# Optimization experiments

Hardware: AMD Instinct MI355X
Metric: run time of the kernel (lower is better)

The kernel has to match this reference:

```python
import jax, jax.numpy as jnp
import numpy as np

EMBED, HID, INSIDE, OUTSIDE, EPS = 128, 64, 4, 8, 1e-5
N_NODES, N_EDGES, BATCH, SEQLEN = 16384, 262144, 64, 21


def _layernorm(x, g, b):
    m = x.mean(-1, keepdims=True)
    v = ((x - m) ** 2).mean(-1, keepdims=True)
    return (x - m) * jax.lax.rsqrt(v + EPS) * g + b


def _lstm_dir(x, Wih, Whh, bih, bhh, reverse):
    # x: [B, L, D] -> h: [B, L, HID]; PyTorch gate order i,f,g,o
    pre = jnp.einsum('bld,gd->blg', x, Wih) + bih + bhh  # [B,L,4H]
    pre = jnp.swapaxes(pre, 0, 1)  # [L,B,4H]
    h0 = jnp.zeros((x.shape[0], HID), x.dtype)

    def step(carry, xt):
        h, c = carry
        gates = xt + h @ Whh.T
        i, f, g, o = jnp.split(gates, 4, axis=-1)
        c = jax.nn.sigmoid(f) * c + jax.nn.sigmoid(i) * jnp.tanh(g)
        h = jax.nn.sigmoid(o) * jnp.tanh(c)
        return (h, c), h

    _, hs = jax.lax.scan(step, (h0, h0), pre, reverse=reverse)
    return jnp.swapaxes(hs, 0, 1)


def setup_inputs():
    key = jax.random.key(0)
    ks = jax.random.split(key, 40)
    f = jnp.float32
    N, E, B, L, D = N_NODES, N_EDGES, BATCH, SEQLEN, EMBED

    def w(k, shape, fan_in):
        return jax.random.normal(k, shape, f) * (1.0 / np.sqrt(fan_in))

    inp = {
        'x': jax.random.normal(ks[0], (N, 2561), f),
        'edge_index': jax.random.randint(ks[1], (2, E), 0, N, jnp.int32),
        'edge_attr': jax.random.normal(ks[2], (E, 3), f),
        # sorted node->graph assignment; every graph id 0..B-1 present
        'batch': ((jnp.arange(N, dtype=jnp.int32) * B) // N).astype(jnp.int32),
        'hotslice': jax.random.normal(ks[3], (B, L, 28), f),
        # randn_like noise tensors from the torch forward, made explicit inputs
        'noise_seqy': jax.random.normal(ks[4], (B, L, D), f),
        'noise_seqz': jax.random.normal(ks[5], (B, L, D), f),
        'noise_sty': jax.random.normal(ks[6], (N, D), f),
        'noise_stz': jax.random.normal(ks[7], (N, D), f),
        # AttnNN params
        'W_esm': w(ks[8], (D, 2560), 2560), 'b_esm': jnp.zeros((D,), f),
        'W_node': w(ks[9], (D, D + 1), D + 1), 'b_node': jnp.zeros((D,), f),
        'W_seq': w(ks[10], (D, 28), 28), 'b_seq': jnp.zeros((D,), f),
        # SeqStructBlock params
        'ln_seq_g': jnp.ones((D,), f), 'ln_seq_b': jnp.zeros((D,), f),
        'ln_st_g': jnp.ones((D,), f), 'ln_st_b': jnp.zeros((D,), f),
        'W_in': w(ks[11], (D, 2 * D + 3), 2 * D + 3), 'b_in': jnp.zeros((D,), f),
        'W_out': w(ks[12], (D, 2 * D + 3), 2 * D + 3), 'b_out': jnp.zeros((D,), f),
        'Wih_f': w(ks[13], (4 * HID, D), HID), 'Whh_f': w(ks[14], (4 * HID, HID), HID),
        'bih_f': jnp.zeros((4 * HID,), f), 'bhh_f': jnp.zeros((4 * HID,), f),
        'Wih_b': w(ks[15], (4 * HID, D), HID), 'Whh_b': w(ks[16], (4 * HID, HID), HID),
        'bih_b': jnp.zeros((4 * HID,), f), 'bhh_b': jnp.zeros((4 * HID,), f),
        # BatchNorm1d (eval mode: running stats)
        'bn_g': jnp.ones((D,), f), 'bn_b': jnp.zeros((D,), f),
        'bn_rm': jnp.zeros((D,), f), 'bn_rv': jnp.ones((D,), f),
    }
    return inp


def reference(x, edge_index, edge_attr, batch, hotslice,
              noise_seqy, noise_seqz, noise_sty, noise_stz,
              W_esm, b_esm, W_node, b_node, W_seq, b_seq,
              ln_seq_g, ln_seq_b, ln_st_g, ln_st_b,
              W_in, b_in, W_out, b_out,
              Wih_f, Whh_f, bih_f, bhh_f, Wih_b, Whh_b, bih_b, bhh_b,
              bn_g, bn_b, bn_rm, bn_rv):
    N = x.shape[0]
    B = hotslice.shape[0]
    src, dst = edge_index[0, 0::2], edge_index[1, 0::2]
    ea_in, ea_out = edge_attr[1::2], edge_attr[0::2]

    def ss(seq, struct):
        # bidirectional LSTM + residual + LayerNorm (dropout = identity, eval)
        hf = _lstm_dir(seq, Wih_f, Whh_f, bih_f, bhh_f, False)
        hb = _lstm_dir(seq, Wih_b, Whh_b, bih_b, bhh_b, True)
        seq = _layernorm(seq + jnp.concatenate([hf, hb], -1), ln_seq_g, ln_seq_b)
        sn = struct
        fs, fd = sn[src], sn[dst]  # [E/2, 128] gathers
        gin = jax.nn.sigmoid(jnp.concatenate([fs, fd, ea_in], -1) @ W_in.T + b_in)
        struct = struct + jax.ops.segment_sum(gin * fd, src, num_segments=N)
        gout = jax.nn.sigmoid(jnp.concatenate([fs, fd, ea_out], -1) @ W_out.T + b_out)
        struct = struct + jax.ops.segment_sum(gout * fs, dst, num_segments=N)
        return seq, _layernorm(struct, ln_st_g, ln_st_b)

    seq0 = hotslice @ W_seq.T + b_seq                       # [B,L,128]
    esm = x[:, 1:] @ W_esm.T + b_esm                        # [N,128]
    struct0 = jnp.concatenate([esm, x[:, :1]], -1) @ W_node.T + b_node  # [N,128]

    def outer(carry):
        sy, sz, ty, tz = carry

        def inner(c, _):
            szc, tzc = c
            return ss(seq0 + sy + szc, struct0 + ty + tzc), None

        (sz, tz), _ = jax.lax.scan(inner, (sz, tz), None, length=INSIDE)
        sy, ty = ss(sy + sz, ty + tz)
        return (sy, sz, ty, tz)

    carry = (noise_seqy, noise_seqz, noise_sty, noise_stz)
    carry, _ = jax.lax.scan(lambda c, _: (outer(c), None), carry, None,
                            length=OUTSIDE - 1)
    sy, sz, ty, tz = outer(carry)

    # middleSelect picks the first node of each consecutive batch run;
    # batch is sorted with every graph id present -> run starts via searchsorted
    starts = jnp.searchsorted(batch, jnp.arange(B, dtype=batch.dtype))
    feat = sy[:, 10, :] + ty[starts]                        # [B,128]
    # BatchNorm1d, eval mode (running stats)
    return (feat - bn_rm) * jax.lax.rsqrt(bn_rv + EPS) * bn_g + bn_b
```

## Files before the change

### kernel.cpp

```cpp
#include <hip/hip_runtime.h>
#include <hip/hip_fp16.h>
#include <math.h>

#define D 128
#define G4 256
#define LSEQ 21
#define EPSF 1e-5f

typedef unsigned short u16;
typedef __attribute__((ext_vector_type(8))) short bf16x8;
typedef __attribute__((ext_vector_type(4))) float f32x4;
typedef __attribute__((ext_vector_type(2))) unsigned u32x2;
typedef __attribute__((ext_vector_type(4))) unsigned u32x4;

#define MFMA16(a,b,c) __builtin_amdgcn_mfma_f32_16x16x32_bf16(a,b,c,0,0,0)

__device__ __forceinline__ float sigf(float x){ return 1.0f/(1.0f+__expf(-x)); }
__device__ __forceinline__ u16 f2bf(float x){
  unsigned u = __float_as_uint(x);
  return (u16)((u + 0x7FFFu + ((u>>16)&1u)) >> 16);
}
__device__ __forceinline__ float bf2f(u16 h){ return __uint_as_float(((unsigned)h)<<16); }
__device__ __forceinline__ unsigned pack_h2(float a, float b){
  __half2 h = __floats2half2_rn(a, b);
  return *(unsigned*)&h;
}
__device__ __forceinline__ float2 unpack_h2(unsigned u){
  __half2 h = *(__half2*)&u;
  return __half22float2(h);
}
__device__ __forceinline__ u16 f2h(float v){ __half h = __float2half(v); return *(u16*)&h; }

__device__ __forceinline__ void edge_acc(u32x4 a, uint2 g, bool valid,
                                         float2 po2, float2 w0, float2 w1, float2 w2,
                                         float& ax, float& ay){
  float e0=__uint_as_float(a.y), e1=__uint_as_float(a.z), e2=__uint_as_float(a.w);
  float2 ps0 = unpack_h2(g.x);
  float2 ps1 = unpack_h2(g.y);
  float gx = po2.x + ps0.x + e0*w0.x + e1*w1.x + e2*w2.x;
  float gy = po2.y + ps1.x + e0*w0.y + e1*w1.y + e2*w2.y;
  float mm = valid ? 1.f : 0.f;
  ax = fmaf(ps0.y*mm, sigf(gx), ax);
  ay = fmaf(ps1.y*mm, sigf(gy), ay);
}

__global__ void k_misc(int* __restrict__ starts, const int* __restrict__ batch, int N, int Bb,
                       float* __restrict__ WEin, float* __restrict__ WEout,
                       const float* __restrict__ W_in, const float* __restrict__ W_out,
                       float* __restrict__ bsum_f, float* __restrict__ bsum_b,
                       const float* __restrict__ bih_f, const float* __restrict__ bhh_f,
                       const float* __restrict__ bih_b, const float* __restrict__ bhh_b){
  int tid = threadIdx.x;
  if (tid < Bb){
    int lo = 0, hi = N;
    while (lo < hi){ int m = (lo+hi)>>1; if (batch[m] < tid) lo = m+1; else hi = m; }
    starts[tid] = lo;
  }
  for (int i = tid; i < 384; i += 256){
    int t = i >> 7, j = i & 127;
    WEin [i] = W_in [(size_t)j*259 + 256 + t];
    WEout[i] = W_out[(size_t)j*259 + 256 + t];
  }
  if (tid < 256){
    bsum_f[tid] = bih_f[tid] + bhh_f[tid];
    bsum_b[tid] = bih_b[tid] + bhh_b[tid];
  }
}

__global__ void k_packB(u16* __restrict__ PB4h, u16* __restrict__ PB4l,
                        u16* __restrict__ PBnh, u16* __restrict__ PBnl,
                        u16* __restrict__ PBEh, u16* __restrict__ PBEl,
                        const float* __restrict__ W_in, const float* __restrict__ W_out,
                        const float* __restrict__ W_node, const float* __restrict__ W_esm){
  int idx = blockIdx.x*256 + threadIdx.x;
  if (idx < 65536){
    int j = idx&7, l=(idx>>3)&63, q=idx>>9;
    int ks = q&3, nt = q>>2;
    int c = nt*16 + (l&15);
    int k = ks*32 + ((l>>4)<<3) + j;
    float v;
    if (c < 128)      v = W_in [(size_t)c*259 + k];
    else if (c < 256) v = W_in [(size_t)(c-128)*259 + 128 + k];
    else if (c < 384) v = W_out[(size_t)(c-256)*259 + k];
    else              v = W_out[(size_t)(c-384)*259 + 128 + k];
    u16 h = f2bf(v);
    PB4h[idx] = h; PB4l[idx] = f2bf(v - bf2f(h));
  } else if (idx < 65536 + 16384){
    int p = idx - 65536;
    int j = p&7, l=(p>>3)&63, q=p>>9;
    int ks = q&3, nt = q>>2;
    int c = nt*16 + (l&15);
    int k = ks*32 + ((l>>4)<<3) + j;
    float v = W_node[(size_t)c*129 + k];
    u16 h = f2bf(v);
    PBnh[p] = h; PBnl[p] = f2bf(v - bf2f(h));
  } else if (idx < 65536 + 16384 + 327680){
    int p = idx - 81920;
    int j = p&7, l=(p>>3)&63, q=p>>9;
    int ks = q%80, nt = q/80;
    int c = nt*16 + (l&15);
    int k = ks*32 + ((l>>4)<<3) + j;
    float v = W_esm[(size_t)c*2560 + k];
    u16 h = f2bf(v);
    PBEh[p] = h; PBEl[p] = f2bf(v - bf2f(h));
  }
}

__global__ void k_seq0(float* __restrict__ seq0, const float* __restrict__ hot,
                       const float* __restrict__ W_seq, const float* __restrict__ b_seq){
  int row = blockIdx.x, j = threadIdx.x;
  const float* h = hot + (size_t)row*28;
  const float* w = W_seq + (size_t)j*28;
  float acc = b_seq[j];
  #pragma unroll
  for (int k = 0; k < 28; k++) acc += h[k]*w[k];
  seq0[(size_t)row*D + j] = acc;
}

__global__ __launch_bounds__(256) void k_esm2(float* __restrict__ struct0, const float* __restrict__ x,
    const u16* __restrict__ PBEh, const u16* __restrict__ PBEl,
    const u16* __restrict__ PBnh, const u16* __restrict__ PBnl,
    const float* __restrict__ b_esm, const float* __restrict__ W_node,
    const float* __restrict__ b_node){
  __shared__ union {
    struct { u16 xh[32*72], xl[32*72]; } p1;
    struct { u16 Ah[32*136], Al[32*136]; } p2;
  } uu;
  __shared__ float esmF[32*132];
  int tid = threadIdx.x;
  int r0 = blockIdx.x*32;
  int w = tid>>6, l = tid&63;
  f32x4 acc[2][2];
  #pragma unroll
  for (int a=0;a<2;a++)
    #pragma unroll
    for (int b=0;b<2;b++) acc[a][b] = (f32x4){0.f,0.f,0.f,0.f};

  float xv[8];
  int rr = tid >> 5, k2i = tid & 31;
  #pragma unroll
  for (int q = 0; q < 4; q++){
    const float* src = x + (size_t)(r0+rr+8*q)*2561 + 1 + k2i*2;
    xv[2*q]   = src[0];
    xv[2*q+1] = src[1];
  }
  for (int kc = 0; kc < 2560; kc += 64){
    __syncthreads();
    unsigned* xh32 = (unsigned*)uu.p1.xh;
    unsigned* xl32 = (unsigned*)uu.p1.xl;
    #pragma unroll
    for (int q = 0; q < 4; q++){
      float v0 = xv[2*q], v1 = xv[2*q+1];
      u16 h0 = f2bf(v0), h1 = f2bf(v1);
      u16 l0 = f2bf(v0 - bf2f(h0)), l1 = f2bf(v1 - bf2f(h1));
      int r = rr + 8*q;
      xh32[r*36 + k2i] = (unsigned)h0 | ((unsigned)h1 << 16);
      xl32[r*36 + k2i] = (unsigned)l0 | ((unsigned)l1 << 16);
    }
    __syncthreads();
    if (kc + 64 < 2560){
      #pragma unroll
      for (int q = 0; q < 4; q++){
        const float* src = x + (size_t)(r0+rr+8*q)*2561 + 1 + kc + 64 + k2i*2;
        xv[2*q]   = src[0];
        xv[2*q+1] = src[1];
      }
    }
    #pragma unroll
    for (int ks = 0; ks < 2; ks++){
      bf16x8 ah[2], al[2];
      #pragma unroll
      for (int rt = 0; rt < 2; rt++){
        int row = rt*16 + (l&15);
        int k = ks*32 + ((l>>4)<<3);
        ah[rt] = *(const bf16x8*)&uu.p1.xh[row*72 + k];
        al[rt] = *(const bf16x8*)&uu.p1.xl[row*72 + k];
      }
      int ksg = (kc>>5) + ks;
      #pragma unroll
      for (int ctl = 0; ctl < 2; ctl++){
        int nt = w*2 + ctl;
        bf16x8 bh = *(const bf16x8*)&PBEh[((size_t)(nt*80 + ksg)*64 + l)*8];
        bf16x8 bl = *(const bf16x8*)&PBEl[((size_t)(nt*80 + ksg)*64 + l)*8];
        #pragma unroll
        for (int rt = 0; rt < 2; rt++){
          acc[rt][ctl] = MFMA16(ah[rt], bh, acc[rt][ctl]);
          acc[rt][ctl] = MFMA16(al[rt], bh, acc[rt][ctl]);
          acc[rt][ctl] = MFMA16(ah[rt], bl, acc[rt][ctl]);
        }
      }
    }
  }
  __syncthreads();
  int cq = l & 15, rqb = (l>>4)*4;
  #pragma unroll
  for (int ctl = 0; ctl < 2; ctl++){
    int coln = (w*2+ctl)*16 + cq;
    float be = b_esm[coln];
    #pragma unroll
    for (int rt = 0; rt < 2; rt++)
      #pragma unroll
      for (int r = 0; r < 4; r++)
        esmF[(rt*16+rqb+r)*132 + coln] = acc[rt][ctl][r] + be;
  }
  __syncthreads();
  {
    unsigned* Ah32 = (unsigned*)uu.p2.Ah;
    unsigned* Al32 = (unsigned*)uu.p2.Al;
    int rr2 = tid >> 6, k2 = tid & 63;
    #pragma unroll
    for (int q = 0; q < 8; q++){
      int r = rr2 + 4*q;
      float v0 = esmF[r*132 + k2*2];
      float v1 = esmF[r*132 + k2*2 + 1];
      u16 h0 = f2bf(v0), h1 = f2bf(v1);
      u16 l0 = f2bf(v0 - bf2f(h0)), l1 = f2bf(v1 - bf2f(h1));
      Ah32[r*68 + k2] = (unsigned)h0 | ((unsigned)h1 << 16);
      Al32[r*68 + k2] = (unsigned)l0 | ((unsigned)l1 << 16);
    }
  }
  __syncthreads();
  f32x4 acc2[2][2];
  #pragma unroll
  for (int a=0;a<2;a++)
    #pragma unroll
    for (int b=0;b<2;b++) acc2[a][b] = (f32x4){0.f,0.f,0.f,0.f};
  #pragma unroll
  for (int ks = 0; ks < 4; ks++){
    bf16x8 ah[2], al[2];
    #pragma unroll
    for (int rt = 0; rt < 2; rt++){
      int row = rt*16 + (l&15);
      int k = ks*32 + ((l>>4)<<3);
      ah[rt] = *(const bf16x8*)&uu.p2.Ah[row*136 + k];
      al[rt] = *(const bf16x8*)&uu.p2.Al[row*136 + k];
    }
    #pragma unroll
    for (int ctl = 0; ctl < 2; ctl++){
      int nt = w*2 + ctl;
      bf16x8 bh = *(const bf16x8*)&PBnh[((size_t)(nt*4 + ks)*64 + l)*8];
      bf16x8 bl = *(const bf16x8*)&PBnl[((size_t)(nt*4 + ks)*64 + l)*8];
      #pragma unroll
      for (int rt = 0; rt < 2; rt++){
        acc2[rt][ctl] = MFMA16(ah[rt], bh, acc2[rt][ctl]);
        acc2[rt][ctl] = MFMA16(al[rt], bh, acc2[rt][ctl]);
        acc2[rt][ctl] = MFMA16(ah[rt], bl, acc2[rt][ctl]);
      }
    }
  }
  #pragma unroll
  for (int ctl = 0; ctl < 2; ctl++){
    int col = (w*2+ctl)*16 + cq;
    float wl = W_node[(size_t)col*129 + 128];
    float bn = b_node[col];
    #pragma unroll
    for (int rt = 0; rt < 2; rt++)
      #pragma unroll
      for (int r = 0; r < 4; r++){
        int row = r0 + rt*16 + rqb + r;
        float x0 = x[(size_t)row*2561];
        struct0[(size_t)row*D + col] = acc2[rt][ctl][r] + x0*wl + bn;
      }
  }
}

__global__ void k_zero2(int* a, int* b, int n){
  int i = blockIdx.x*blockDim.x + threadIdx.x;
  if (i < n){ a[i] = 0; b[i] = 0; }
}
__global__ void k_count(int* cnt_s, int* cnt_d, const int* __restrict__ ei, int E2){
  int e = blockIdx.x*blockDim.x + threadIdx.x;
  if (e < E2){
    atomicAdd(&cnt_s[ei[2*e]], 1);
    atomicAdd(&cnt_d[ei[2*E2 + 2*e]], 1);
  }
}
__global__ __launch_bounds__(1024) void k_scan(const int* __restrict__ cnt, int* __restrict__ offs, int n){
  __shared__ int sh[1024];
  __shared__ int sbase;
  int tid = threadIdx.x;
  if (tid == 0) sbase = 0;
  __syncthreads();
  for (int chunk = 0; chunk < n; chunk += 1024){
    int v = (chunk+tid < n) ? cnt[chunk+tid] : 0;
    sh[tid] = v;
    __syncthreads();
    for (int off = 1; off < 1024; off <<= 1){
      int t = (tid >= off) ? sh[tid-off] : 0;
      __syncthreads();
      sh[tid] += t;
      __syncthreads();
    }
    if (chunk+tid < n) offs[chunk+tid] = sbase + sh[tid] - v;
    __syncthreads();
    if (tid == 0) sbase += sh[1023];
    __syncthreads();
  }
  if (tid == 0) offs[n] = sbase;
}
__global__ void k_copy2(int* cur_s, const int* offs_s, int* cur_d, const int* offs_d, int n){
  int i = blockIdx.x*blockDim.x + threadIdx.x;
  if (i < n){ cur_s[i] = offs_s[i]; cur_d[i] = offs_d[i]; }
}
__global__ void k_fill(const int* __restrict__ ei, const float* __restrict__ eattr, int E2,
                       int* cur_s, int4* __restrict__ adj_s,
                       int* cur_d, int4* __restrict__ adj_d){
  int e = blockIdx.x*blockDim.x + threadIdx.x;
  if (e >= E2) return;
  int s = ei[2*e];
  int d = ei[2*E2 + 2*e];
  const float* ein  = eattr + (size_t)(2*e+1)*3;
  const float* eout = eattr + (size_t)(2*e)*3;
  int ps = atomicAdd(&cur_s[s], 1);
  adj_s[ps] = make_int4(d, __float_as_int(ein[0]),  __float_as_int(ein[1]),  __float_as_int(ein[2]));
  int pd = atomicAdd(&cur_d[d], 1);
  adj_d[pd] = make_int4(s, __float_as_int(eout[0]), __float_as_int(eout[1]), __float_as_int(eout[2]));
}
__global__ void k_pad(int4* __restrict__ adj_s, int4* __restrict__ adj_d, int E2){
  int t = threadIdx.x;
  if (t < 8){
    adj_s[E2+t] = make_int4(0,0,0,0);
    adj_d[E2+t] = make_int4(0,0,0,0);
  }
}

__global__ __launch_bounds__(256) void k_A(
  const float* __restrict__ s0t, const float* __restrict__ ty, const float* __restrict__ tz,
  float* __restrict__ struct_in,
  const u16* __restrict__ PB4h, const u16* __restrict__ PB4l,
  unsigned* __restrict__ G_in, unsigned* __restrict__ G_out,
  unsigned* __restrict__ PownPk,
  const float* __restrict__ b_in, const float* __restrict__ b_out,
  const float* __restrict__ s0s, const float* __restrict__ sy, const float* __restrict__ sz,
  float* __restrict__ seq_in, float* __restrict__ pre_f, float* __restrict__ pre_b,
  const float* __restrict__ Wih_f, const float* __restrict__ Wih_b,
  const float* __restrict__ bsum_f, const float* __restrict__ bsum_b,
  int N, int Bb)
{
  __shared__ union {
    struct { u16 Ah[32*136], Al[32*136]; float Sf[32*132]; } m;
    float sh[LSEQ*128];
  } u;
  int tid = threadIdx.x;
  if ((int)blockIdx.x >= Bb){
    int r0 = (blockIdx.x - Bb)*32;
    const float4* ty4 = (const float4*)(ty + (size_t)r0*D);
    const float4* tz4 = (const float4*)(tz + (size_t)r0*D);
    const float4* s04 = s0t ? (const float4*)(s0t + (size_t)r0*D) : nullptr;
    float4* si4 = (float4*)(struct_in + (size_t)r0*D);
    #pragma unroll
    for (int q = 0; q < 4; q++){
      int i = tid + 256*q;
      int r = i >> 5, k4 = i & 31;
      float4 v = ty4[i];
      float4 z = tz4[i];
      v.x += z.x; v.y += z.y; v.z += z.z; v.w += z.w;
      if (s04){ float4 s = s04[i]; v.x += s.x; v.y += s.y; v.z += s.z; v.w += s.w; }
      si4[i] = v;
      u16 h0 = f2bf(v.x), h1 = f2bf(v.y), h2 = f2bf(v.z), h3 = f2bf(v.w);
      *(ushort4*)&u.m.Ah[r*136 + k4*4] = make_ushort4(h0,h1,h2,h3);
      *(ushort4*)&u.m.Al[r*136 + k4*4] = make_ushort4(
          f2bf(v.x - bf2f(h0)), f2bf(v.y - bf2f(h1)),
          f2bf(v.z - bf2f(h2)), f2bf(v.w - bf2f(h3)));
      *(float4*)&u.m.Sf[r*132 + k4*4] = v;
    }
    __syncthreads();
    int w = tid >> 6, l = tid & 63;
    f32x4 acc[2][8];
    #pragma unroll
    for (int a=0;a<2;a++)
      #pragma unroll
      for (int b=0;b<8;b++) acc[a][b] = (f32x4){0.f,0.f,0.f,0.f};
    #pragma unroll
    for (int ks = 0; ks < 4; ks++){
      bf16x8 ah[2], al[2];
      #pragma unroll
      for (int rt = 0; rt < 2; rt++){
        int row = rt*16 + (l&15);
        int k = ks*32 + ((l>>4)<<3);
        ah[rt] = *(const bf16x8*)&u.m.Ah[row*136 + k];
        al[rt] = *(const bf16x8*)&u.m.Al[row*136 + k];
      }
      #pragma unroll
      for (int ct = 0; ct < 8; ct++){
        int nt = w*8 + ct;
        bf16x8 bh = *(const bf16x8*)&PB4h[((size_t)(nt*4 + ks)*64 + l)*8];
        bf16x8 bl = *(const bf16x8*)&PB4l[((size_t)(nt*4 + ks)*64 + l)*8];
        #pragma unroll
        for (int rt = 0; rt < 2; rt++){
          acc[rt][ct] = MFMA16(ah[rt], bh, acc[rt][ct]);
          acc[rt][ct] = MFMA16(al[rt], bh, acc[rt][ct]);
          acc[rt][ct] = MFMA16(ah[rt], bl, acc[rt][ct]);
        }
      }
    }
    __syncthreads();
    unsigned* stg = (unsigned*)u.m.Ah;
    u16* stg16 = (u16*)u.m.Ah;
    int cq = l & 15, rqb = (l>>4)*4;
    if (w == 1){
      #pragma unroll
      for (int ct = 0; ct < 8; ct++){
        int coln = ct*16 + cq;
        #pragma unroll
        for (int rt = 0; rt < 2; rt++){
          #pragma unroll
          for (int r = 0; r < 4; r++){
            int lr = rt*16 + rqb + r;
            stg[lr*128 + coln] = pack_h2(acc[rt][ct][r], u.m.Sf[lr*132 + coln]);
          }
        }
      }
    }
    __syncthreads();
    {
      uint4* dst = (uint4*)(G_in + (size_t)r0*D);
      const uint4* src = (const uint4*)stg;
      #pragma unroll
      for (int q = 0; q < 4; q++) dst[tid + 256*q] = src[tid + 256*q];
    }
    __syncthreads();
    if (w == 2){
      #pragma unroll
      for (int ct = 0; ct < 8; ct++){
        int coln = ct*16 + cq;
        #pragma unroll
        for (int rt = 0; rt < 2; rt++){
          #pragma unroll
          for (int r = 0; r < 4; r++){
            int lr = rt*16 + rqb + r;
            stg[lr*128 + coln] = pack_h2(acc[rt][ct][r], u.m.Sf[lr*132 + coln]);
          }
        }
      }
    }
    __syncthreads();
    {
      uint4* dst = (uint4*)(G_out + (size_t)r0*D);
      const uint4* src = (const uint4*)stg;
      #pragma unroll
      for (int q = 0; q < 4; q++) dst[tid + 256*q] = src[tid + 256*q];
    }
    __syncthreads();
    if (w == 0 || w == 3){
      const float* bb = (w == 0) ? b_in : b_out;
      int half = (w == 0) ? 0 : 1;
      #pragma unroll
      for (int ct = 0; ct < 8; ct++){
        int coln = ct*16 + cq;
        float bc = bb[coln];
        #pragma unroll
        for (int rt = 0; rt < 2; rt++){
          #pragma unroll
          for (int r = 0; r < 4; r++){
            int lr = rt*16 + rqb + r;
            stg16[(lr*128 + coln)*2 + half] = f2h(acc[rt][ct][r] + bc);
          }
        }
      }
    }
    __syncthreads();
    {
      uint4* dst = (uint4*)(PownPk + (size_t)r0*D);
      const uint4* src = (const uint4*)stg;
      #pragma unroll
      for (int q = 0; q < 4; q++) dst[tid + 256*q] = src[tid + 256*q];
    }
  } else {
    int b = blockIdx.x;
    for (int idx = tid; idx < LSEQ*128; idx += 256){
      size_t off = (size_t)b*LSEQ*128 + idx;
      float v = sy[off] + sz[off];
      if (s0s) v += s0s[off];
      u.sh[idx] = v;
      seq_in[off] = v;
    }
    __syncthreads();
    int g = tid;
    float accf[LSEQ], accb[LSEQ];
    float bf = bsum_f[g], bb = bsum_b[g];
    #pragma unroll
    for (int l = 0; l < LSEQ; l++){ accf[l] = bf; accb[l] = bb; }
    const float* wfp = Wih_f + (size_t)g*128;
    const float* wbp = Wih_b + (size_t)g*128;
    for (int kc = 0; kc < 128; kc += 16){
      float4 wf[4], wb[4];
      #pragma unroll
      for (int q = 0; q < 4; q++){
        wf[q] = *(const float4*)(wfp + kc + 4*q);
        wb[q] = *(const float4*)(wbp + kc + 4*q);
      }
      #pragma unroll
      for (int l = 0; l < LSEQ; l++){
        #pragma unroll
        for (int q = 0; q < 4; q++){
          float4 s4 = *(const float4*)&u.sh[l*128 + kc + 4*q];
          accf[l] += s4.x*wf[q].x + s4.y*wf[q].y + s4.z*wf[q].z + s4.w*wf[q].w;
          accb[l] += s4.x*wb[q].x + s4.y*wb[q].y + s4.z*wb[q].z + s4.w*wb[q].w;
        }
      }
    }
    for (int l = 0; l < LSEQ; l++){
      pre_f[((size_t)b*LSEQ + l)*G4 + g] = accf[l];
      pre_b[((size_t)b*LSEQ + l)*G4 + g] = accb[l];
    }
  }
}

__global__ __launch_bounds__(512) void k_B(
  const unsigned* __restrict__ G_in, const unsigned* __restrict__ G_out,
  const unsigned* __restrict__ PownPk,
  const float* __restrict__ struct_in, float* __restrict__ struct_out,
  const int* __restrict__ offs_s, const int4* __restrict__ adj_s,
  const int* __restrict__ offs_d, const int4* __restrict__ adj_d,
  const float* __restrict__ WEin, const float* __restrict__ WEout,
  const float* __restrict__ ln_st_g, const float* __restrict__ ln_st_b,
  const float* __restrict__ pre_f, const float* __restrict__ pre_b,
  const float* __restrict__ Whh_f, const float* __restrict__ Whh_b,
  const float* __restrict__ seq_in, float* __restrict__ seq_out,
  const float* __restrict__ ln_seq_g, const float* __restrict__ ln_seq_b,
  int N, int Bb)
{
  __shared__ float h_hist[2][LSEQ][64];
  __shared__ float hcur[2][64];
  __shared__ float gsh[2][G4];
  if ((int)blockIdx.x >= Bb){
    int wv = threadIdx.x >> 6, lane = threadIdx.x & 63;
    int n0 = ((blockIdx.x - Bb)*8 + wv)*4;
    const float2* WEi2 = (const float2*)WEin;
    const float2* WEo2 = (const float2*)WEout;
    float2 wi0 = WEi2[lane], wi1 = WEi2[64+lane], wi2 = WEi2[128+lane];
    float2 wo0 = WEo2[lane], wo1 = WEo2[64+lane], wo2 = WEo2[128+lane];
    float2 g2v = ((const float2*)ln_st_g)[lane], be2 = ((const float2*)ln_st_b)[lane];
    const uint2* Gi = (const uint2*)G_in;
    const uint2* Go = (const uint2*)G_out;
    #pragma unroll 1
    for (int n = n0; n < n0+4; ++n){
      u32x2 pw = *((const u32x2*)PownPk + (size_t)n*64 + lane);
      float2 pp0 = unpack_h2(pw.x), pp1 = unpack_h2(pw.y);
      float2 poI = make_float2(pp0.x, pp1.x);
      float2 poO = make_float2(pp0.y, pp1.y);
      float ax = 0.f, ay = 0.f;
      int j0 = __builtin_amdgcn_readfirstlane(offs_s[n]);
      int j1 = __builtin_amdgcn_readfirstlane(offs_s[n+1]);
      for (int jb = j0; jb < j1; jb += 4){
        int rem = j1 - jb;
        const u32x4* ap = (const u32x4*)adj_s + jb;
        u32x4 a0 = ap[0], a1 = ap[1], a2 = ap[2], a3 = ap[3];
        uint2 g0 = Gi[(size_t)a0.x*64 + lane];
        uint2 g1 = Gi[(size_t)a1.x*64 + lane];
        uint2 g2 = Gi[(size_t)a2.x*64 + lane];
        uint2 g3 = Gi[(size_t)a3.x*64 + lane];
        edge_acc(a0, g0, true,  poI, wi0, wi1, wi2, ax, ay);
        edge_acc(a1, g1, rem>1, poI, wi0, wi1, wi2, ax, ay);
        edge_acc(a2, g2, rem>2, poI, wi0, wi1, wi2, ax, ay);
        edge_acc(a3, g3, rem>3, poI, wi0, wi1, wi2, ax, ay);
      }
      j0 = __builtin_amdgcn_readfirstlane(offs_d[n]);
      j1 = __builtin_amdgcn_readfirstlane(offs_d[n+1]);
      for (int jb = j0; jb < j1; jb += 4){
        int rem = j1 - jb;
        const u32x4* ap = (const u32x4*)adj_d + jb;
        u32x4 a0 = ap[0], a1 = ap[1], a2 = ap[2], a3 = ap[3];
        uint2 g0 = Go[(size_t)a0.x*64 + lane];
        uint2 g1 = Go[(size_t)a1.x*64 + lane];
        uint2 g2 = Go[(size_t)a2.x*64 + lane];
        uint2 g3 = Go[(size_t)a3.x*64 + lane];
        edge_acc(a0, g0, true,  poO, wo0, wo1, wo2, ax, ay);
        edge_acc(a1, g1, rem>1, poO, wo0, wo1, wo2, ax, ay);
        edge_acc(a2, g2, rem>2, poO, wo0, wo1, wo2, ax, ay);
        edge_acc(a3, g3, rem>3, poO, wo0, wo1, wo2, ax, ay);
      }
      float2 sn = ((const float2*)struct_in)[(size_t)n*64 + lane];
      float vx = sn.x + ax;
      float vy = sn.y + ay;
      float s = vx+vy, sq = vx*vx + vy*vy;
      #pragma unroll
      for (int o = 32; o; o >>= 1){ s += __shfl_xor(s, o); sq += __shfl_xor(sq, o); }
      float mean = s*(1.f/128.f);
      float inv = rsqrtf(sq*(1.f/128.f) - mean*mean + EPSF);
      float2 o2;
      o2.x = (vx-mean)*inv*g2v.x + be2.x;
      o2.y = (vy-mean)*inv*g2v.y + be2.y;
      ((float2*)struct_out)[(size_t)n*64 + lane] = o2;
    }
  } else {
    int b = blockIdx.x;
    int tid = threadIdx.x;
    int dir = tid >> 8, g = tid & 255;
    const float* Whh = dir ? Whh_b : Whh_f;
    const float* pre = dir ? pre_b : pre_f;
    float w[64];
    #pragma unroll
    for (int q = 0; q < 16; q++){
      float4 t4 = *(const float4*)(Whh + (size_t)g*64 + 4*q);
      w[4*q] = t4.x; w[4*q+1] = t4.y; w[4*q+2] = t4.z; w[4*q+3] = t4.w;
    }
    float c = 0.f;
    for (int t = 0; t < LSEQ; ++t){
      int tt = dir ? (LSEQ-1-t) : t;
      float gate = pre[((size_t)b*LSEQ + tt)*G4 + g];
      if (t > 0){
        #pragma unroll
        for (int q = 0; q < 16; q++){
          float4 h4 = *(const float4*)&hcur[dir][4*q];
          gate += w[4*q]*h4.x + w[4*q+1]*h4.y + w[4*q+2]*h4.z + w[4*q+3]*h4.w;
        }
      }
      gsh[dir][g] = gate;
      __syncthreads();
      if (g < 64){
        float iv = gsh[dir][g], fv = gsh[dir][64+g], gv = gsh[dir][128+g], ov = gsh[dir][192+g];
        c = sigf(fv)*c + sigf(iv)*tanhf(gv);
        float h = sigf(ov)*tanhf(c);
        hcur[dir][g] = h;
        h_hist[dir][tt][g] = h;
      }
      __syncthreads();
    }
    int wv = tid >> 6, lane = tid & 63;
    for (int l = wv; l < LSEQ; l += 8){
      float2 sv = ((const float2*)(seq_in + ((size_t)b*LSEQ + l)*128))[lane];
      float hv0, hv1;
      if (lane < 32){ hv0 = h_hist[0][l][2*lane];    hv1 = h_hist[0][l][2*lane+1]; }
      else          { hv0 = h_hist[1][l][2*lane-64]; hv1 = h_hist[1][l][2*lane-63]; }
      float vx = sv.x + hv0, vy = sv.y + hv1;
      float s = vx+vy, sq = vx*vx + vy*vy;
      #pragma unroll
      for (int o = 32; o; o >>= 1){ s += __shfl_xor(s, o); sq += __shfl_xor(sq, o); }
      float mean = s*(1.f/128.f);
      float inv = rsqrtf(sq*(1.f/128.f) - mean*mean + EPSF);
      float2 g2 = ((const float2*)ln_seq_g)[lane], b2 = ((const float2*)ln_seq_b)[lane];
      float2 o2;
      o2.x = (vx-mean)*inv*g2.x + b2.x;
      o2.y = (vy-mean)*inv*g2.y + b2.y;
      ((float2*)(seq_out + ((size_t)b*LSEQ + l)*128))[lane] = o2;
    }
  }
}

__global__ void k_final(float* __restrict__ out, const float* __restrict__ sy,
                        const float* __restrict__ ty, const int* __restrict__ starts,
                        const float* __restrict__ g, const float* __restrict__ b,
                        const float* __restrict__ rm, const float* __restrict__ rv, int Bb){
  int i = blockIdx.x*blockDim.x + threadIdx.x;
  if (i >= Bb*D) return;
  int bb = i >> 7, d = i & 127;
  float feat = sy[((size_t)bb*LSEQ + 10)*D + d] + ty[(size_t)starts[bb]*D + d];
  out[i] = (feat - rm[d])*rsqrtf(rv[d]+EPSF)*g[d] + b[d];
}

extern "C" void kernel_launch(void* const* d_in, const int* in_sizes, int n_in,
                              void* d_out, int out_size, void* d_ws, size_t ws_size,
                              hipStream_t stream)
{
  const float* x        = (const float*)d_in[0];
  const int*   ei       = (const int*)  d_in[1];
  const float* eattr    = (const float*)d_in[2];
  const int*   batch    = (const int*)  d_in[3];
  const float* hotslice = (const float*)d_in[4];
  const float* nsy      = (const float*)d_in[5];
  const float* nsz      = (const float*)d_in[6];
  const float* nty      = (const float*)d_in[7];
  const float* ntz      = (const float*)d_in[8];
  const float* W_esm    = (const float*)d_in[9];
  const float* b_esm    = (const float*)d_in[10];
  const float* W_node   = (const float*)d_in[11];
  const float* b_node   = (const float*)d_in[12];
  const float* W_seq    = (const float*)d_in[13];
  const float* b_seq    = (const float*)d_in[14];
  const float* ln_seq_g = (const float*)d_in[15];
  const float* ln_seq_b = (const float*)d_in[16];
  const float* ln_st_g  = (const float*)d_in[17];
  const float* ln_st_b  = (const float*)d_in[18];
  const float* W_in     = (const float*)d_in[19];
  const float* b_in     = (const float*)d_in[20];
  const float* W_out    = (const float*)d_in[21];
  const float* b_out    = (const float*)d_in[22];
  const float* Wih_f    = (const float*)d_in[23];
  const float* Whh_f    = (const float*)d_in[24];
  const float* bih_f    = (const float*)d_in[25];
  const float* bhh_f    = (const float*)d_in[26];
  const float* Wih_b    = (const float*)d_in[27];
  const float* Whh_b    = (const float*)d_in[28];
  const float* bih_b    = (const float*)d_in[29];
  const float* bhh_b    = (const float*)d_in[30];
  const float* bn_g     = (const float*)d_in[31];
  const float* bn_b     = (const float*)d_in[32];
  const float* bn_rm    = (const float*)d_in[33];
  const float* bn_rv    = (const float*)d_in[34];

  const int N  = in_sizes[0] / 2561;
  const int E  = in_sizes[1] / 2;
  const int E2 = E / 2;
  const int Bb = in_sizes[4] / (LSEQ*28);
  const int BL = Bb*LSEQ;

  char* p = (char*)d_ws;
  auto alloc = [&](size_t bytes)->void*{
    void* r = (void*)p; p += (bytes + 255) & ~(size_t)255; return r;
  };
  float*    seq0      = (float*)alloc((size_t)BL*D*4);
  float*    sy        = (float*)alloc((size_t)BL*D*4);
  float*    sz        = (float*)alloc((size_t)BL*D*4);
  float*    seq_in    = (float*)alloc((size_t)BL*D*4);
  float*    pre_f     = (float*)alloc((size_t)BL*G4*4);
  float*    pre_b     = (float*)alloc((size_t)BL*G4*4);
  float*    struct0   = (float*)alloc((size_t)N*D*4);
  float*    ty        = (float*)alloc((size_t)N*D*4);
  float*    tz        = (float*)alloc((size_t)N*D*4);
  float*    struct_in = (float*)alloc((size_t)N*D*4);
  unsigned* G_in      = (unsigned*)alloc((size_t)N*D*4);
  unsigned* G_out     = (unsigned*)alloc((size_t)N*D*4);
  unsigned* PownPk    = (unsigned*)alloc((size_t)N*D*4);
  u16*      PB4h      = (u16*)alloc(65536*2);
  u16*      PB4l      = (u16*)alloc(65536*2);
  u16*      PBnh      = (u16*)alloc(16384*2);
  u16*      PBnl      = (u16*)alloc(16384*2);
  u16*      PBEh      = (u16*)alloc(327680*2);
  u16*      PBEl      = (u16*)alloc(327680*2);
  float*    WEin      = (float*)alloc(384*4);
  float*    WEout     = (float*)alloc(384*4);
  float*    bsum_f    = (float*)alloc(256*4);
  float*    bsum_b    = (float*)alloc(256*4);
  int*      starts    = (int*)alloc((size_t)Bb*4);
  int*      cnt_s     = (int*)alloc((size_t)N*4);
  int*      cnt_d     = (int*)alloc((size_t)N*4);
  int*      offs_s    = (int*)alloc((size_t)(N+1)*4);
  int*      offs_d    = (int*)alloc((size_t)(N+1)*4);
  int*      cur_s     = (int*)alloc((size_t)N*4);
  int*      cur_d     = (int*)alloc((size_t)N*4);
  int4*     adj_s     = (int4*)alloc((size_t)(E2+8)*16);
  int4*     adj_d     = (int4*)alloc((size_t)(E2+8)*16);
  (void)ws_size; (void)n_in; (void)out_size;

  hipMemcpyAsync(sy, nsy, (size_t)BL*D*4, hipMemcpyDeviceToDevice, stream);
  hipMemcpyAsync(sz, nsz, (size_t)BL*D*4, hipMemcpyDeviceToDevice, stream);
  hipMemcpyAsync(ty, nty, (size_t)N*D*4, hipMemcpyDeviceToDevice, stream);
  hipMemcpyAsync(tz, ntz, (size_t)N*D*4, hipMemcpyDeviceToDevice, stream);

  k_misc<<<1, 256, 0, stream>>>(starts, batch, N, Bb, WEin, WEout, W_in, W_out,
                                bsum_f, bsum_b, bih_f, bhh_f, bih_b, bhh_b);
  k_packB<<<1600, 256, 0, stream>>>(PB4h, PB4l, PBnh, PBnl, PBEh, PBEl,
                                    W_in, W_out, W_node, W_esm);
  k_seq0<<<BL, 128, 0, stream>>>(seq0, hotslice, W_seq, b_seq);
  k_esm2<<<N/32, 256, 0, stream>>>(struct0, x, PBEh, PBEl, PBnh, PBnl,
                                   b_esm, W_node, b_node);
  k_zero2<<<(N+255)/256, 256, 0, stream>>>(cnt_s, cnt_d, N);
  k_count<<<(E2+255)/256, 256, 0, stream>>>(cnt_s, cnt_d, ei, E2);
  k_scan<<<1, 1024, 0, stream>>>(cnt_s, offs_s, N);
  k_scan<<<1, 1024, 0, stream>>>(cnt_d, offs_d, N);
  k_copy2<<<(N+255)/256, 256, 0, stream>>>(cur_s, offs_s, cur_d, offs_d, N);
  k_fill<<<(E2+255)/256, 256, 0, stream>>>(ei, eattr, E2, cur_s, adj_s, cur_d, adj_d);
  k_pad<<<1, 64, 0, stream>>>(adj_s, adj_d, E2);

  const int NB_T1 = N/32;
  const int NB_T2 = N/32;

  for (int o = 0; o < 8; ++o){
    for (int it = 0; it < 5; ++it){
      bool inner = (it < 4);
      const float* s0s = inner ? seq0 : nullptr;
      const float* s0t = inner ? struct0 : nullptr;
      float* so = inner ? sz : sy;
      float* to = inner ? tz : ty;
      k_A<<<Bb + NB_T1, 256, 0, stream>>>(s0t, ty, tz, struct_in, PB4h, PB4l,
                                          G_in, G_out, PownPk, b_in, b_out,
                                          s0s, sy, sz, seq_in, pre_f, pre_b,
                                          Wih_f, Wih_b, bsum_f, bsum_b, N, Bb);
      k_B<<<Bb + NB_T2, 512, 0, stream>>>(G_in, G_out, PownPk, struct_in, to,
                                          offs_s, adj_s, offs_d, adj_d,
                                          WEin, WEout, ln_st_g, ln_st_b,
                                          pre_f, pre_b, Whh_f, Whh_b, seq_in, so,
                                          ln_seq_g, ln_seq_b, N, Bb);
    }
  }

  k_final<<<(Bb*D+255)/256, 256, 0, stream>>>((float*)d_out, sy, ty, starts,
                                              bn_g, bn_b, bn_rm, bn_rv, Bb);
}
```

Measured before the change: 4.360 ms.

## Drop struct_in buffer, reuse packed G_in residual, double-buffer ESM staging

The separate fp32 struct_in buffer is removed. k_B now takes the residual value from the fp16 half already packed into G_in, which saves a full N×128 fp32 write and read every iteration. k_A stages G_in and G_out into two separate LDS regions so both can be written out in one pass with fewer barriers, at the cost of extra shared memory. The one-time ESM GEMM gets a double-buffered LDS pipeline for its x tiles. The risks are lower residual precision from the fp16 value and possibly lower occupancy in k_A from the larger LDS footprint.

```diff
diff --git a/kernel.cpp b/kernel.cpp
--- a/kernel.cpp
+++ b/kernel.cpp
@@ -123,7 +123,7 @@
     const float* __restrict__ b_esm, const float* __restrict__ W_node,
     const float* __restrict__ b_node){
   __shared__ union {
-    struct { u16 xh[32*72], xl[32*72]; } p1;
+    struct { u16 xh[2][32*72], xl[2][32*72]; } p1;
     struct { u16 Ah[32*136], Al[32*136]; } p2;
   } uu;
   __shared__ float esmF[32*132];
@@ -136,36 +136,39 @@
     #pragma unroll
     for (int b=0;b<2;b++) acc[a][b] = (f32x4){0.f,0.f,0.f,0.f};
 
-  float xv[8];
   int rr = tid >> 5, k2i = tid & 31;
-  #pragma unroll
-  for (int q = 0; q < 4; q++){
-    const float* src = x + (size_t)(r0+rr+8*q)*2561 + 1 + k2i*2;
-    xv[2*q]   = src[0];
-    xv[2*q+1] = src[1];
-  }
-  for (int kc = 0; kc < 2560; kc += 64){
-    __syncthreads();
-    unsigned* xh32 = (unsigned*)uu.p1.xh;
-    unsigned* xl32 = (unsigned*)uu.p1.xl;
+  float xv[8], xw[8];
+  auto loadx = [&](float* dst, int kc){
     #pragma unroll
     for (int q = 0; q < 4; q++){
-      float v0 = xv[2*q], v1 = xv[2*q+1];
+      const float* src = x + (size_t)(r0+rr+8*q)*2561 + 1 + kc + k2i*2;
+      dst[2*q]   = src[0];
+      dst[2*q+1] = src[1];
+    }
+  };
+  auto stage = [&](const float* vv, int buf){
+    unsigned* xh32 = (unsigned*)uu.p1.xh[buf];
+    unsigned* xl32 = (unsigned*)uu.p1.xl[buf];
+    #pragma unroll
+    for (int q = 0; q < 4; q++){
+      float v0 = vv[2*q], v1 = vv[2*q+1];
       u16 h0 = f2bf(v0), h1 = f2bf(v1);
       u16 l0 = f2bf(v0 - bf2f(h0)), l1 = f2bf(v1 - bf2f(h1));
       int r = rr + 8*q;
       xh32[r*36 + k2i] = (unsigned)h0 | ((unsigned)h1 << 16);
       xl32[r*36 + k2i] = (unsigned)l0 | ((unsigned)l1 << 16);
     }
-    __syncthreads();
-    if (kc + 64 < 2560){
-      #pragma unroll
-      for (int q = 0; q < 4; q++){
-        const float* src = x + (size_t)(r0+rr+8*q)*2561 + 1 + kc + 64 + k2i*2;
-        xv[2*q]   = src[0];
-        xv[2*q+1] = src[1];
-      }
-    }
+  };
+  loadx(xv, 0);
+  loadx(xw, 64);
+  stage(xv, 0);
+  #pragma unroll
+  for (int q = 0; q < 8; q++) xv[q] = xw[q];
+  loadx(xw, 128);
+  __syncthreads();
+  int cur = 0;
+  for (int kc = 0; kc < 2560; kc += 64){
+    if (kc + 64 < 2560) stage(xv, cur^1);
     #pragma unroll
     for (int ks = 0; ks < 2; ks++){
       bf16x8 ah[2], al[2];
@@ -173,8 +176,8 @@
       for (int rt = 0; rt < 2; rt++){
         int row = rt*16 + (l&15);
         int k = ks*32 + ((l>>4)<<3);
-        ah[rt] = *(const bf16x8*)&uu.p1.xh[row*72 + k];
-        al[rt] = *(const bf16x8*)&uu.p1.xl[row*72 + k];
+        ah[rt] = *(const bf16x8*)&uu.p1.xh[cur][row*72 + k];
+        al[rt] = *(const bf16x8*)&uu.p1.xl[cur][row*72 + k];
       }
       int ksg = (kc>>5) + ks;
       #pragma unroll
@@ -190,8 +193,12 @@
         }
       }
     }
-  }
-  __syncthreads();
+    #pragma unroll
+    for (int q = 0; q < 8; q++) xv[q] = xw[q];
+    if (kc + 192 < 2560) loadx(xw, kc + 192);
+    __syncthreads();
+    cur ^= 1;
+  }
   int cq = l & 15, rqb = (l>>4)*4;
   #pragma unroll
   for (int ctl = 0; ctl < 2; ctl++){
@@ -326,7 +333,6 @@
 
 __global__ __launch_bounds__(256) void k_A(
   const float* __restrict__ s0t, const float* __restrict__ ty, const float* __restrict__ tz,
-  float* __restrict__ struct_in,
   const u16* __restrict__ PB4h, const u16* __restrict__ PB4l,
   unsigned* __restrict__ G_in, unsigned* __restrict__ G_out,
   unsigned* __restrict__ PownPk,
@@ -338,7 +344,7 @@
   int N, int Bb)
 {
   __shared__ union {
-    struct { u16 Ah[32*136], Al[32*136]; float Sf[32*132]; } m;
+    struct { u16 Ah[32*136], Al[32*136]; float Sf[32*132]; unsigned stg2[32*128]; } m;
     float sh[LSEQ*128];
   } u;
   int tid = threadIdx.x;
@@ -347,7 +353,6 @@
     const float4* ty4 = (const float4*)(ty + (size_t)r0*D);
     const float4* tz4 = (const float4*)(tz + (size_t)r0*D);
     const float4* s04 = s0t ? (const float4*)(s0t + (size_t)r0*D) : nullptr;
-    float4* si4 = (float4*)(struct_in + (size_t)r0*D);
     #pragma unroll
     for (int q = 0; q < 4; q++){
       int i = tid + 256*q;
@@ -356,7 +361,6 @@
       float4 z = tz4[i];
       v.x += z.x; v.y += z.y; v.z += z.z; v.w += z.w;
       if (s04){ float4 s = s04[i]; v.x += s.x; v.y += s.y; v.z += s.z; v.w += s.w; }
-      si4[i] = v;
       u16 h0 = f2bf(v.x), h1 = f2bf(v.y), h2 = f2bf(v.z), h3 = f2bf(v.w);
       *(ushort4*)&u.m.Ah[r*136 + k4*4] = make_ushort4(h0,h1,h2,h3);
       *(ushort4*)&u.m.Al[r*136 + k4*4] = make_ushort4(
@@ -395,54 +399,46 @@
       }
     }
     __syncthreads();
-    unsigned* stg = (unsigned*)u.m.Ah;
-    u16* stg16 = (u16*)u.m.Ah;
+    unsigned* stg1 = (unsigned*)u.m.Ah;
+    unsigned* stg2 = u.m.stg2;
     int cq = l & 15, rqb = (l>>4)*4;
     if (w == 1){
       #pragma unroll
       for (int ct = 0; ct < 8; ct++){
         int coln = ct*16 + cq;
         #pragma unroll
-        for (int rt = 0; rt < 2; rt++){
+        for (int rt = 0; rt < 2; rt++)
           #pragma unroll
           for (int r = 0; r < 4; r++){
             int lr = rt*16 + rqb + r;
-            stg[lr*128 + coln] = pack_h2(acc[rt][ct][r], u.m.Sf[lr*132 + coln]);
+            stg1[lr*128 + coln] = pack_h2(acc[rt][ct][r], u.m.Sf[lr*132 + coln]);
           }
-        }
-      }
-    }
-    __syncthreads();
-    {
-      uint4* dst = (uint4*)(G_in + (size_t)r0*D);
-      const uint4* src = (const uint4*)stg;
-      #pragma unroll
-      for (int q = 0; q < 4; q++) dst[tid + 256*q] = src[tid + 256*q];
-    }
-    __syncthreads();
-    if (w == 2){
+      }
+    } else if (w == 2){
       #pragma unroll
       for (int ct = 0; ct < 8; ct++){
         int coln = ct*16 + cq;
         #pragma unroll
-        for (int rt = 0; rt < 2; rt++){
+        for (int rt = 0; rt < 2; rt++)
           #pragma unroll
           for (int r = 0; r < 4; r++){
             int lr = rt*16 + rqb + r;
-            stg[lr*128 + coln] = pack_h2(acc[rt][ct][r], u.m.Sf[lr*132 + coln]);
+            stg2[lr*128 + coln] = pack_h2(acc[rt][ct][r], u.m.Sf[lr*132 + coln]);
           }
-        }
       }
     }
     __syncthreads();
     {
-      uint4* dst = (uint4*)(G_out + (size_t)r0*D);
-      const uint4* src = (const uint4*)stg;
-      #pragma unroll
-      for (int q = 0; q < 4; q++) dst[tid + 256*q] = src[tid + 256*q];
+      int grp = w >> 1;
+      uint4* dst = grp ? (uint4*)(G_out + (size_t)r0*D) : (uint4*)(G_in + (size_t)r0*D);
+      const uint4* src = grp ? (const uint4*)stg2 : (const uint4*)stg1;
+      int base = (w & 1)*64 + l;
+      #pragma unroll
+      for (int q = 0; q < 8; q++) dst[base + 128*q] = src[base + 128*q];
     }
     __syncthreads();
     if (w == 0 || w == 3){
+      u16* stgPk16 = (u16*)stg1;
       const float* bb = (w == 0) ? b_in : b_out;
       int half = (w == 0) ? 0 : 1;
       #pragma unroll
@@ -450,19 +446,18 @@
         int coln = ct*16 + cq;
         float bc = bb[coln];
         #pragma unroll
-        for (int rt = 0; rt < 2; rt++){
+        for (int rt = 0; rt < 2; rt++)
           #pragma unroll
           for (int r = 0; r < 4; r++){
             int lr = rt*16 + rqb + r;
-            stg16[(lr*128 + coln)*2 + half] = f2h(acc[rt][ct][r] + bc);
+            stgPk16[(lr*128 + coln)*2 + half] = f2h(acc[rt][ct][r] + bc);
           }
-        }
       }
     }
     __syncthreads();
     {
       uint4* dst = (uint4*)(PownPk + (size_t)r0*D);
-      const uint4* src = (const uint4*)stg;
+      const uint4* src = (const uint4*)stg1;
       #pragma unroll
       for (int q = 0; q < 4; q++) dst[tid + 256*q] = src[tid + 256*q];
     }
@@ -510,7 +505,7 @@
 __global__ __launch_bounds__(512) void k_B(
   const unsigned* __restrict__ G_in, const unsigned* __restrict__ G_out,
   const unsigned* __restrict__ PownPk,
-  const float* __restrict__ struct_in, float* __restrict__ struct_out,
+  float* __restrict__ struct_out,
   const int* __restrict__ offs_s, const int4* __restrict__ adj_s,
   const int* __restrict__ offs_d, const int4* __restrict__ adj_d,
   const float* __restrict__ WEin, const float* __restrict__ WEout,
@@ -540,6 +535,7 @@
       float2 pp0 = unpack_h2(pw.x), pp1 = unpack_h2(pw.y);
       float2 poI = make_float2(pp0.x, pp1.x);
       float2 poO = make_float2(pp0.y, pp1.y);
+      uint2 gown = Gi[(size_t)n*64 + lane];
       float ax = 0.f, ay = 0.f;
       int j0 = __builtin_amdgcn_readfirstlane(offs_s[n]);
       int j1 = __builtin_amdgcn_readfirstlane(offs_s[n+1]);
@@ -571,9 +567,8 @@
         edge_acc(a2, g2, rem>2, poO, wo0, wo1, wo2, ax, ay);
         edge_acc(a3, g3, rem>3, poO, wo0, wo1, wo2, ax, ay);
       }
-      float2 sn = ((const float2*)struct_in)[(size_t)n*64 + lane];
-      float vx = sn.x + ax;
-      float vy = sn.y + ay;
+      float vx = unpack_h2(gown.x).y + ax;
+      float vy = unpack_h2(gown.y).y + ay;
       float s = vx+vy, sq = vx*vx + vy*vy;
       #pragma unroll
       for (int o = 32; o; o >>= 1){ s += __shfl_xor(s, o); sq += __shfl_xor(sq, o); }
@@ -709,7 +704,6 @@
   float*    struct0   = (float*)alloc((size_t)N*D*4);
   float*    ty        = (float*)alloc((size_t)N*D*4);
   float*    tz        = (float*)alloc((size_t)N*D*4);
-  float*    struct_in = (float*)alloc((size_t)N*D*4);
   unsigned* G_in      = (unsigned*)alloc((size_t)N*D*4);
   unsigned* G_out     = (unsigned*)alloc((size_t)N*D*4);
   unsigned* PownPk    = (unsigned*)alloc((size_t)N*D*4);
@@ -764,11 +758,11 @@
       const float* s0t = inner ? struct0 : nullptr;
       float* so = inner ? sz : sy;
       float* to = inner ? tz : ty;
-      k_A<<<Bb + NB_T1, 256, 0, stream>>>(s0t, ty, tz, struct_in, PB4h, PB4l,
+      k_A<<<Bb + NB_T1, 256, 0, stream>>>(s0t, ty, tz, PB4h, PB4l,
                                           G_in, G_out, PownPk, b_in, b_out,
                                           s0s, sy, sz, seq_in, pre_f, pre_b,
                                           Wih_f, Wih_b, bsum_f, bsum_b, N, Bb);
-      k_B<<<Bb + NB_T2, 512, 0, stream>>>(G_in, G_out, PownPk, struct_in, to,
+      k_B<<<Bb + NB_T2, 512, 0, stream>>>(G_in, G_out, PownPk, to,
                                           offs_s, adj_s, offs_d, adj_d,
                                           WEin, WEout, ln_st_g, ln_st_b,
                                           pre_f, pre_b, Whh_f, Whh_b, seq_in, so,
```

Measured after the change: 4.280 ms. Within noise of the previous version (-1.8%).
